# Performance work log

Hardware: AMD Instinct MI355X
Metric: run time of the kernel (lower is better)

## Reference

```python
import jax, jax.numpy as jnp
import numpy as np

B, L, C = 8, 8192, 512

def setup_inputs() -> dict:
    key = jax.random.key(0)
    kq, kk, kv_, kw = jax.random.split(key, 4)
    q = jax.random.normal(kq, (B, L, C), dtype=jnp.float32)
    k = jax.random.normal(kk, (B, L, C), dtype=jnp.float32)
    v = jax.random.normal(kv_, (B, L, C), dtype=jnp.float32)
    W = jax.random.normal(kw, (C, C), dtype=jnp.float32) * (1.0 / np.sqrt(C))
    b = jnp.zeros((C,), dtype=jnp.float32)
    return {"q": q, "k": k, "v": v, "W": W, "b": b}

def reference(q, k, v, W, b):
    # L2-normalize q and k over channel dim (matches torch x / x.norm(dim=-1, keepdim=True))
    qn = q / jnp.linalg.norm(q, axis=-1, keepdims=True)
    kn = k / jnp.linalg.norm(k, axis=-1, keepdims=True)
    # kv = k * v, dropout is identity (p=0 / eval); global sum over sequence
    kv_sum = jnp.sum(kn * v, axis=-2, keepdims=True)  # [B, 1, C]
    out = kv_sum * qn                                  # [B, L, C]
    # output Linear: out @ W^T + b (torch nn.Linear convention, W:[out,in])
    return jnp.einsum('blc,oc->blo', out, W) + b
```

## Files before the change

### kernel.cpp

```cpp
#include <hip/hip_runtime.h>
#include <hip/hip_bf16.h>
#include <stdint.h>

#define B_ 8
#define L_ 8192
#define C_ 512

typedef short bf16x8 __attribute__((ext_vector_type(8)));
typedef float f32x4 __attribute__((ext_vector_type(4)));

#define GAS(p) ((const __attribute__((address_space(1))) void*)(p))
#define LAS(p) ((__attribute__((address_space(3))) void*)(p))

__global__ __launch_bounds__(256)
void kv_qnorm(const float* __restrict__ kin, const float* __restrict__ vin,
              const float* __restrict__ qin, float* __restrict__ kv,
              __hip_bfloat16* __restrict__ qb) {
    const int bi   = blockIdx.x;
    const int b    = bi >> 8;
    const int row0 = (bi & 255) * 32;
    const int lane = threadIdx.x & 63;
    const int wave = threadIdx.x >> 6;

    const f32x4* kb = (const f32x4*)(kin + ((size_t)b * L_ + row0) * C_);
    const f32x4* vb = (const f32x4*)(vin + ((size_t)b * L_ + row0) * C_);

    f32x4 acca = {0.f,0.f,0.f,0.f}, accb = {0.f,0.f,0.f,0.f};

    #pragma unroll 1
    for (int it = 0; it < 2; ++it) {
        const int r0 = wave * 8 + it * 4;
        f32x4 ka[4], kc[4], va[4], vc[4];
        #pragma unroll
        for (int j = 0; j < 4; ++j) {
            const f32x4* krow = kb + (size_t)(r0 + j) * (C_/4);
            ka[j] = __builtin_nontemporal_load(krow + lane);
            kc[j] = __builtin_nontemporal_load(krow + 64 + lane);
        }
        #pragma unroll
        for (int j = 0; j < 4; ++j) {
            const f32x4* vrow = vb + (size_t)(r0 + j) * (C_/4);
            va[j] = __builtin_nontemporal_load(vrow + lane);
            vc[j] = __builtin_nontemporal_load(vrow + 64 + lane);
        }
        float ss[4];
        #pragma unroll
        for (int j = 0; j < 4; ++j)
            ss[j] = ka[j][0]*ka[j][0] + ka[j][1]*ka[j][1] + ka[j][2]*ka[j][2] + ka[j][3]*ka[j][3]
                  + kc[j][0]*kc[j][0] + kc[j][1]*kc[j][1] + kc[j][2]*kc[j][2] + kc[j][3]*kc[j][3];
        #pragma unroll
        for (int m = 32; m >= 1; m >>= 1) {
            #pragma unroll
            for (int j = 0; j < 4; ++j) ss[j] += __shfl_xor(ss[j], m);
        }
        #pragma unroll
        for (int j = 0; j < 4; ++j) {
            const float inv = rsqrtf(ss[j]);
            #pragma unroll
            for (int x = 0; x < 4; ++x) {
                acca[x] += ka[j][x] * inv * va[j][x];
                accb[x] += kc[j][x] * inv * vc[j][x];
            }
        }
    }

    const f32x4* qg = (const f32x4*)(qin + ((size_t)b * L_ + row0) * C_);
    __hip_bfloat16* qbo = qb + ((size_t)b * L_ + row0) * C_;
    #pragma unroll 1
    for (int it = 0; it < 2; ++it) {
        const int r0 = wave * 8 + it * 4;
        f32x4 qa[4], qc[4];
        #pragma unroll
        for (int j = 0; j < 4; ++j) {
            const f32x4* qrow = qg + (size_t)(r0 + j) * (C_/4);
            qa[j] = __builtin_nontemporal_load(qrow + lane);
            qc[j] = __builtin_nontemporal_load(qrow + 64 + lane);
        }
        float ss[4];
        #pragma unroll
        for (int j = 0; j < 4; ++j)
            ss[j] = qa[j][0]*qa[j][0] + qa[j][1]*qa[j][1] + qa[j][2]*qa[j][2] + qa[j][3]*qa[j][3]
                  + qc[j][0]*qc[j][0] + qc[j][1]*qc[j][1] + qc[j][2]*qc[j][2] + qc[j][3]*qc[j][3];
        #pragma unroll
        for (int m = 32; m >= 1; m >>= 1) {
            #pragma unroll
            for (int j = 0; j < 4; ++j) ss[j] += __shfl_xor(ss[j], m);
        }
        #pragma unroll
        for (int j = 0; j < 4; ++j) {
            const float inv = rsqrtf(ss[j]);
            union { __hip_bfloat16 h[4]; uint2 u; } p0, p1;
            p0.h[0] = __float2bfloat16(qa[j][0] * inv);
            p0.h[1] = __float2bfloat16(qa[j][1] * inv);
            p0.h[2] = __float2bfloat16(qa[j][2] * inv);
            p0.h[3] = __float2bfloat16(qa[j][3] * inv);
            p1.h[0] = __float2bfloat16(qc[j][0] * inv);
            p1.h[1] = __float2bfloat16(qc[j][1] * inv);
            p1.h[2] = __float2bfloat16(qc[j][2] * inv);
            p1.h[3] = __float2bfloat16(qc[j][3] * inv);
            uint2* dst = (uint2*)(qbo + (size_t)(r0 + j) * C_);
            dst[lane]      = p0.u;
            dst[64 + lane] = p1.u;
        }
    }

    __shared__ __align__(16) float red[4][C_];
    ((f32x4*)&red[wave][0])[lane]      = acca;
    ((f32x4*)&red[wave][0])[64 + lane] = accb;
    __syncthreads();
    for (int c = threadIdx.x; c < C_; c += 256) {
        float s = red[0][c] + red[1][c] + red[2][c] + red[3][c];
        atomicAdd(&kv[b * C_ + c], s);
    }
}

__global__ __launch_bounds__(256)
void prep_w(const float* __restrict__ W, const float* __restrict__ kv,
            __hip_bfloat16* __restrict__ Wb) {
    int idx = blockIdx.x * 256 + threadIdx.x;
    int e   = idx << 2;
    int b   = e >> 18;
    int oc  = e & 0x3FFFF;
    int c   = oc & (C_ - 1);
    float4 w4 = *(const float4*)(W + oc);
    float4 s4 = *(const float4*)(kv + b * C_ + c);
    union { __hip_bfloat16 h[4]; uint2 u; } pk;
    pk.h[0] = __float2bfloat16(w4.x * s4.x);
    pk.h[1] = __float2bfloat16(w4.y * s4.y);
    pk.h[2] = __float2bfloat16(w4.z * s4.z);
    pk.h[3] = __float2bfloat16(w4.w * s4.w);
    *(uint2*)(Wb + e) = pk.u;
}

__global__ __launch_bounds__(256, 2)
void gemm_out(const __hip_bfloat16* __restrict__ qbin, const __hip_bfloat16* __restrict__ Wb,
              const float* __restrict__ bias, float* __restrict__ out) {
    const int blk   = blockIdx.x;
    const int xcd   = blk & 7;
    const int local = blk >> 3;
    const int n0    = (local & 3) * 128;
    const int m0    = (xcd * 64 + (local >> 2)) * 128;
    const int b     = m0 >> 13;
    const int tid  = threadIdx.x;
    const int lane = tid & 63;
    const int wave = tid >> 6;

    __shared__ __align__(16) unsigned short As[2][128 * 64];
    __shared__ __align__(16) unsigned short Bs[2][128 * 64];

    const __hip_bfloat16* Abase = qbin + (size_t)m0 * C_;
    const __hip_bfloat16* Bbase = Wb + ((size_t)b * C_ + n0) * C_;

    const int r16 = lane & 15;
    const int qd  = lane >> 4;
    const int wm  = wave & 1;
    const int wn  = wave >> 1;

    f32x4 acc[4][4];
    #pragma unroll
    for (int i = 0; i < 4; ++i)
        #pragma unroll
        for (int j = 0; j < 4; ++j)
            acc[i][j] = (f32x4){0.f, 0.f, 0.f, 0.f};

    auto stage = [&](int buf, int kc) {
        #pragma unroll
        for (int i = 0; i < 4; ++i) {
            int cid = i * 256 + wave * 64 + lane;
            int r   = cid >> 3;
            int cj  = cid & 7;
            int kk  = ((cj ^ (r & 7)) << 3);
            __builtin_amdgcn_global_load_lds(GAS(Abase + (size_t)r * C_ + kc + kk),
                LAS(&As[buf][(i * 256 + wave * 64) * 8]), 16, 0, 0);
            __builtin_amdgcn_global_load_lds(GAS(Bbase + (size_t)r * C_ + kc + kk),
                LAS(&Bs[buf][(i * 256 + wave * 64) * 8]), 16, 0, 0);
        }
    };
    auto compute = [&](int buf) {
        #pragma unroll
        for (int ks = 0; ks < 2; ++ks) {
            bf16x8 af[4], bfr[4];
            #pragma unroll
            for (int t = 0; t < 4; ++t) {
                int m = wm * 64 + t * 16 + r16;
                af[t]  = *(const bf16x8*)&As[buf][m * 64 + (((ks * 4 + qd) ^ (m & 7)) << 3)];
                int n = wn * 64 + t * 16 + r16;
                bfr[t] = *(const bf16x8*)&Bs[buf][n * 64 + (((ks * 4 + qd) ^ (n & 7)) << 3)];
            }
            #pragma unroll
            for (int mt = 0; mt < 4; ++mt)
                #pragma unroll
                for (int nt = 0; nt < 4; ++nt)
                    acc[mt][nt] = __builtin_amdgcn_mfma_f32_16x16x32_bf16(
                        af[mt], bfr[nt], acc[mt][nt], 0, 0, 0);
        }
    };

    stage(0, 0);
    __syncthreads();
    #pragma unroll
    for (int t = 0; t < 7; ++t) {
        stage((t & 1) ^ 1, (t + 1) * 64);
        compute(t & 1);
        __syncthreads();
    }
    compute(1);

    #pragma unroll
    for (int nt = 0; nt < 4; ++nt) {
        int col  = n0 + wn * 64 + nt * 16 + r16;
        float bv = bias[col];
        #pragma unroll
        for (int mt = 0; mt < 4; ++mt) {
            int rl = wm * 64 + mt * 16 + qd * 4;
            float* op = out + (size_t)(m0 + rl) * C_ + col;
            op[0]      = acc[mt][nt][0] + bv;
            op[C_]     = acc[mt][nt][1] + bv;
            op[2 * C_] = acc[mt][nt][2] + bv;
            op[3 * C_] = acc[mt][nt][3] + bv;
        }
    }
}

extern "C" void kernel_launch(void* const* d_in, const int* in_sizes, int n_in,
                              void* d_out, int out_size, void* d_ws, size_t ws_size,
                              hipStream_t stream) {
    const float* q    = (const float*)d_in[0];
    const float* k    = (const float*)d_in[1];
    const float* v    = (const float*)d_in[2];
    const float* W    = (const float*)d_in[3];
    const float* bias = (const float*)d_in[4];
    float* out = (float*)d_out;

    float* kv = (float*)d_ws;
    __hip_bfloat16* Wb = (__hip_bfloat16*)((char*)d_ws + 16384);
    __hip_bfloat16* qb = (__hip_bfloat16*)((char*)d_ws + 16384 + (size_t)B_ * C_ * C_ * 2);

    hipMemsetAsync(kv, 0, B_ * C_ * sizeof(float), stream);
    kv_qnorm<<<2048, 256, 0, stream>>>(k, v, q, kv, qb);
    prep_w<<<2048, 256, 0, stream>>>(W, kv, Wb);
    gemm_out<<<2048, 256, 0, stream>>>(qb, Wb, bias, out);
}
```

Baseline: 412.9 us.

## Enlarge GEMM tile to 256x256 with 8 waves and barrier-interleaved MFMA phases

The output GEMM now uses 256x256 tiles computed by 512-thread blocks, with each wave holding an 8x4 grid of 16x16 MFMA accumulators. This raises data reuse per LDS load and halves the grid along each dimension. Each K chunk is split into two phases with an s_barrier and setprio around the MFMA burst, so the waves stay in step. The 128 KB of LDS and the larger accumulator set reduce occupancy, and 512 blocks may leave fewer waves available to hide latency.

```diff
diff --git a/kernel.cpp b/kernel.cpp
--- a/kernel.cpp
+++ b/kernel.cpp
@@ -132,33 +132,32 @@
     *(uint2*)(Wb + e) = pk.u;
 }
 
-__global__ __launch_bounds__(256, 2)
+__global__ __launch_bounds__(512, 2)
 void gemm_out(const __hip_bfloat16* __restrict__ qbin, const __hip_bfloat16* __restrict__ Wb,
               const float* __restrict__ bias, float* __restrict__ out) {
     const int blk   = blockIdx.x;
     const int xcd   = blk & 7;
     const int local = blk >> 3;
-    const int n0    = (local & 3) * 128;
-    const int m0    = (xcd * 64 + (local >> 2)) * 128;
-    const int b     = m0 >> 13;
-    const int tid  = threadIdx.x;
-    const int lane = tid & 63;
-    const int wave = tid >> 6;
-
-    __shared__ __align__(16) unsigned short As[2][128 * 64];
-    __shared__ __align__(16) unsigned short Bs[2][128 * 64];
+    const int n0    = (local & 1) * 256;
+    const int m0    = (xcd * 32 + (local >> 1)) * 256;
+    const int b     = xcd;
+    const int tid   = threadIdx.x;
+    const int lane  = tid & 63;
+    const int wave  = tid >> 6;
+    const int wn    = wave & 3;
+    const int wm    = wave >> 2;
+    const int r16   = lane & 15;
+    const int qd    = lane >> 4;
+
+    __shared__ __align__(16) unsigned short As[2][256 * 64];
+    __shared__ __align__(16) unsigned short Bs[2][256 * 64];
 
     const __hip_bfloat16* Abase = qbin + (size_t)m0 * C_;
     const __hip_bfloat16* Bbase = Wb + ((size_t)b * C_ + n0) * C_;
 
-    const int r16 = lane & 15;
-    const int qd  = lane >> 4;
-    const int wm  = wave & 1;
-    const int wn  = wave >> 1;
-
-    f32x4 acc[4][4];
+    f32x4 acc[8][4];
     #pragma unroll
-    for (int i = 0; i < 4; ++i)
+    for (int i = 0; i < 8; ++i)
         #pragma unroll
         for (int j = 0; j < 4; ++j)
             acc[i][j] = (f32x4){0.f, 0.f, 0.f, 0.f};
@@ -166,58 +165,62 @@
     auto stage = [&](int buf, int kc) {
         #pragma unroll
         for (int i = 0; i < 4; ++i) {
-            int cid = i * 256 + wave * 64 + lane;
-            int r   = cid >> 3;
-            int cj  = cid & 7;
-            int kk  = ((cj ^ (r & 7)) << 3);
-            __builtin_amdgcn_global_load_lds(GAS(Abase + (size_t)r * C_ + kc + kk),
-                LAS(&As[buf][(i * 256 + wave * 64) * 8]), 16, 0, 0);
-            __builtin_amdgcn_global_load_lds(GAS(Bbase + (size_t)r * C_ + kc + kk),
-                LAS(&Bs[buf][(i * 256 + wave * 64) * 8]), 16, 0, 0);
+            const int cb = (wave * 4 + i) * 64;
+            const int r  = (cb >> 3) + (lane >> 3);
+            const int gk = (((lane & 7) ^ (r & 7)) << 3);
+            __builtin_amdgcn_global_load_lds(GAS(Abase + (size_t)r * C_ + kc + gk),
+                LAS(&As[buf][cb * 8]), 16, 0, 0);
+            __builtin_amdgcn_global_load_lds(GAS(Bbase + (size_t)r * C_ + kc + gk),
+                LAS(&Bs[buf][cb * 8]), 16, 0, 0);
         }
     };
-    auto compute = [&](int buf) {
-        #pragma unroll
-        for (int ks = 0; ks < 2; ++ks) {
-            bf16x8 af[4], bfr[4];
-            #pragma unroll
-            for (int t = 0; t < 4; ++t) {
-                int m = wm * 64 + t * 16 + r16;
-                af[t]  = *(const bf16x8*)&As[buf][m * 64 + (((ks * 4 + qd) ^ (m & 7)) << 3)];
-                int n = wn * 64 + t * 16 + r16;
-                bfr[t] = *(const bf16x8*)&Bs[buf][n * 64 + (((ks * 4 + qd) ^ (n & 7)) << 3)];
-            }
-            #pragma unroll
-            for (int mt = 0; mt < 4; ++mt)
-                #pragma unroll
-                for (int nt = 0; nt < 4; ++nt)
-                    acc[mt][nt] = __builtin_amdgcn_mfma_f32_16x16x32_bf16(
-                        af[mt], bfr[nt], acc[mt][nt], 0, 0, 0);
-        }
+
+    auto phase = [&](int buf, int ks) {
+        bf16x8 af[8], bfr[4];
+        #pragma unroll
+        for (int i = 0; i < 8; ++i) {
+            const int row = wm * 128 + i * 16 + r16;
+            af[i] = *(const bf16x8*)&As[buf][row * 64 + ((((ks << 2) | qd) ^ (row & 7)) << 3)];
+        }
+        #pragma unroll
+        for (int j = 0; j < 4; ++j) {
+            const int row = wn * 64 + j * 16 + r16;
+            bfr[j] = *(const bf16x8*)&Bs[buf][row * 64 + ((((ks << 2) | qd) ^ (row & 7)) << 3)];
+        }
+        __builtin_amdgcn_sched_barrier(0);
+        __builtin_amdgcn_s_barrier();
+        __builtin_amdgcn_s_setprio(1);
+        #pragma unroll
+        for (int i = 0; i < 8; ++i)
+            #pragma unroll
+            for (int j = 0; j < 4; ++j)
+                acc[i][j] = __builtin_amdgcn_mfma_f32_16x16x32_bf16(
+                    af[i], bfr[j], acc[i][j], 0, 0, 0);
+        __builtin_amdgcn_s_setprio(0);
     };
 
     stage(0, 0);
     __syncthreads();
     #pragma unroll
-    for (int t = 0; t < 7; ++t) {
-        stage((t & 1) ^ 1, (t + 1) * 64);
-        compute(t & 1);
-        __syncthreads();
-    }
-    compute(1);
+    for (int t = 0; t < 8; ++t) {
+        if (t < 7) stage((t + 1) & 1, (t + 1) * 64);
+        phase(t & 1, 0);
+        phase(t & 1, 1);
+        if (t < 7) __syncthreads();
+    }
 
     #pragma unroll
-    for (int nt = 0; nt < 4; ++nt) {
-        int col  = n0 + wn * 64 + nt * 16 + r16;
-        float bv = bias[col];
-        #pragma unroll
-        for (int mt = 0; mt < 4; ++mt) {
-            int rl = wm * 64 + mt * 16 + qd * 4;
-            float* op = out + (size_t)(m0 + rl) * C_ + col;
-            op[0]      = acc[mt][nt][0] + bv;
-            op[C_]     = acc[mt][nt][1] + bv;
-            op[2 * C_] = acc[mt][nt][2] + bv;
-            op[3 * C_] = acc[mt][nt][3] + bv;
+    for (int j = 0; j < 4; ++j) {
+        const int col = n0 + wn * 64 + j * 16 + r16;
+        const float bv = bias[col];
+        #pragma unroll
+        for (int i = 0; i < 8; ++i) {
+            const int rl = m0 + wm * 128 + i * 16 + qd * 4;
+            float* op = out + (size_t)rl * C_ + col;
+            op[0]      = acc[i][j][0] + bv;
+            op[C_]     = acc[i][j][1] + bv;
+            op[2 * C_] = acc[i][j][2] + bv;
+            op[3 * C_] = acc[i][j][3] + bv;
         }
     }
 }
@@ -239,5 +242,5 @@
     hipMemsetAsync(kv, 0, B_ * C_ * sizeof(float), stream);
     kv_qnorm<<<2048, 256, 0, stream>>>(k, v, q, kv, qb);
     prep_w<<<2048, 256, 0, stream>>>(W, kv, Wb);
-    gemm_out<<<2048, 256, 0, stream>>>(qb, Wb, bias, out);
-}
+    gemm_out<<<512, 512, 0, stream>>>(qb, Wb, bias, out);
+}
```

Result: slower. 431.7 us (+4.5%).
